# Kernel optimization log

Measured on AMD Instinct MI355X. Metric: run time of the kernel, lower is better.

Reference implementation:

```python
import jax, jax.numpy as jnp
import numpy as np

MARGIN = 0.3
WARMUP_EPOCHS = 10
K = 5
ALPHA = 2.0
SAME_CAM_NEG_BOOST = 1.2
NEG_INF = jnp.float32(-jnp.inf)
POS_INF = jnp.float32(jnp.inf)


def setup_inputs() -> dict:
    key = jax.random.key(0)
    k1, k2, k3 = jax.random.split(key, 3)
    N, D = 8192, 2048
    feats = jax.random.normal(k1, (N, D), dtype=jnp.float32)
    labels = jax.random.randint(k2, (N,), 0, 256, dtype=jnp.int64)
    camids = jax.random.randint(k3, (N,), 0, 8, dtype=jnp.int64)
    return {"feats": feats, "labels": labels, "camids": camids, "epoch": 20}


def _topk_mean(dist_mat, mask, k, largest):
    # dist_mat [N,N], mask [N,N] bool. Per-row mean of k largest/smallest valid elems.
    if largest:
        work = jnp.where(mask, dist_mat, NEG_INF)
        vals, _ = jax.lax.top_k(work, k)            # [N,k] largest
        fallback = jnp.max(work, axis=1)
    else:
        work = jnp.where(mask, dist_mat, POS_INF)
        vals = -jax.lax.top_k(-work, k)[0]          # [N,k] smallest
        fallback = jnp.min(work, axis=1)
    is_valid = jnp.isfinite(vals)
    safe_sum = jnp.sum(jnp.where(is_valid, vals, 0.0), axis=1)
    counts = jnp.maximum(is_valid.sum(axis=1), 1)
    mean = safe_sum / counts
    return jnp.where(is_valid.any(axis=1), mean, fallback)


def _forward(feats, labels, camids, epoch):
    # (1) L2 normalize
    norm = jnp.linalg.norm(feats, axis=-1, keepdims=True)
    x = feats / jnp.maximum(norm, 1e-12)
    # Euclidean distance matrix [N,N]
    sq = jnp.sum(x * x, axis=1)
    dist2 = sq[:, None] + sq[None, :] - 2.0 * (x @ x.T)
    dist = jnp.sqrt(jnp.maximum(dist2, 1e-12))
    # masks (constants w.r.t. grad)
    N = feats.shape[0]
    eye = jnp.eye(N, dtype=bool)
    same_label = labels[:, None] == labels[None, :]
    same_cam = camids[:, None] == camids[None, :]
    is_pos = same_label & ~eye & ~same_cam   # cross_cam_pos=True
    is_neg = ~same_label & ~eye
    # boosted same-camera negatives
    neg_bias = jnp.where(is_neg & same_cam, SAME_CAM_NEG_BOOST, 1.0)
    dist_neg_sel = dist / jnp.maximum(neg_bias, 1e-6)
    # (2) top-k hard mining
    d_ap = _topk_mean(dist, is_pos, K, largest=True)
    d_an = _topk_mean(dist_neg_sel, is_neg, K, largest=False)
    # (5) hardness-aware weighting (no grad)
    w = jax.lax.stop_gradient(jax.nn.sigmoid(ALPHA * (d_ap - d_an)))
    w = w / jnp.maximum(w.mean(), 1e-12)
    # (3) margin schedule
    if epoch is not None and epoch < WARMUP_EPOCHS:
        per_sample = jax.nn.softplus(-(d_an - d_ap))
    else:
        per_sample = jax.nn.relu(d_ap - d_an + MARGIN)  # MarginRankingLoss, y=1
    loss = jnp.mean(w * per_sample)
    return loss, jax.lax.stop_gradient(d_ap), jax.lax.stop_gradient(d_an)


def reference(feats, labels, camids, epoch):
    return _forward(feats, labels, camids, epoch)
```

## Files before the change

kernel.cpp:

```cpp
#include <hip/hip_runtime.h>
#include <hip/hip_bf16.h>
#include <stdint.h>

typedef float   floatx4  __attribute__((ext_vector_type(4)));
typedef float   floatx16 __attribute__((ext_vector_type(16)));
typedef int     intx4    __attribute__((ext_vector_type(4)));
typedef int     intx8    __attribute__((ext_vector_type(8)));
typedef _Float16 halfx8  __attribute__((ext_vector_type(8)));
typedef _Float16 halfx4  __attribute__((ext_vector_type(4)));
typedef _Float16 half2v  __attribute__((ext_vector_type(2)));

#define NROW 8192
#define NDIM 2048
#define BM 128
#define SLICE 64
#define NSLICE 32
#define NSTRIP 64
#define NTILE (NSTRIP*(NSTRIP+1)/2)
#define NPOSB 256
#define DT_LD 136
#define KL_SYM 64
#define SLOT_P 8
#define MERGE_BLOCKS 256
#define BOOST_INV 0.6944444444f
#define XBT_STRIP 262144
#define XBT_SLICE 8192

__device__ __forceinline__ void ins_desc(float (&a)[5], float v) {
#pragma unroll
    for (int k = 0; k < 5; ++k) { float hi = fmaxf(a[k], v); float lo = fminf(a[k], v); a[k] = hi; v = lo; }
}
__device__ __forceinline__ void ins_asc(float (&a)[5], float v) {
#pragma unroll
    for (int k = 0; k < 5; ++k) { float lo = fminf(a[k], v); float hi = fmaxf(a[k], v); a[k] = lo; v = hi; }
}

__device__ __forceinline__ int   h2bits(half2v v) { return __builtin_bit_cast(int, v); }
__device__ __forceinline__ half2v bits2h(int v)   { return __builtin_bit_cast(half2v, v); }
__device__ __forceinline__ void ins_desc2(half2v (&a)[5], half2v v) {
#pragma unroll
    for (int k = 0; k < 5; ++k) {
        half2v hi = __builtin_elementwise_max(a[k], v);
        half2v lo = __builtin_elementwise_min(a[k], v);
        a[k] = hi; v = lo;
    }
}
__device__ __forceinline__ void ins_asc2(half2v (&a)[5], half2v v) {
#pragma unroll
    for (int k = 0; k < 5; ++k) {
        half2v lo = __builtin_elementwise_min(a[k], v);
        half2v hi = __builtin_elementwise_max(a[k], v);
        a[k] = lo; v = hi;
    }
}

__device__ __forceinline__ void load_lds16(const void* g, void* l) {
    __builtin_amdgcn_global_load_lds((__attribute__((address_space(1))) void*)(void*)g,
                                     (__attribute__((address_space(3))) void*)l,
                                     16, 0, 0);
}

__global__ __launch_bounds__(256) void k_normalize(const float* __restrict__ feats,
                                                   unsigned char* __restrict__ xb,
                                                   unsigned char* __restrict__ xbt,
                                                   float* __restrict__ sq) {
    const int lane = threadIdx.x & 63;
    const int row = (blockIdx.x << 2) + (threadIdx.x >> 6);
    const float* f = feats + (size_t)row * NDIM;
    float4 v[8];
    float ss = 0.f;
#pragma unroll
    for (int i = 0; i < 8; ++i) {
        v[i] = *(const float4*)(f + ((i << 6) + lane) * 4);
        ss += v[i].x * v[i].x + v[i].y * v[i].y + v[i].z * v[i].z + v[i].w * v[i].w;
    }
#pragma unroll
    for (int o = 32; o > 0; o >>= 1) ss += __shfl_xor(ss, o);
    float inv = 1.0f / fmaxf(sqrtf(ss), 1e-12f);
    if (lane == 0) sq[row] = ss * inv * inv;
    unsigned char* xo = xb + (size_t)row * NDIM;
    const int strip = row >> 7, rr = row & 127, g = rr >> 5, m32r = rr & 31;
    unsigned char* bt = xbt + (size_t)strip * XBT_STRIP + g * 2048 + m32r * 32
                      + ((lane >> 4) * XBT_SLICE) + (((lane >> 3) & 1) * 1024) + 4 * (lane & 7);
#pragma unroll
    for (int i = 0; i < 8; ++i) {
        int w0 = __builtin_amdgcn_cvt_pk_fp8_f32(v[i].x * inv, v[i].y * inv, 0, false);
        w0     = __builtin_amdgcn_cvt_pk_fp8_f32(v[i].z * inv, v[i].w * inv, w0, true);
        *(int*)(xo + ((i << 6) + lane) * 4) = w0;
        *(int*)(bt + (size_t)4 * i * XBT_SLICE) = w0;
    }
}

__device__ __forceinline__ void scan_half_row_neg(const _Float16* Dt_,
        int srow, int shalf, float (&neg5)[5]) {
    const int s2 = 2 * (srow & 7);
    const int PINF2 = 0x7C007C00;
    half2v n5[5];
#pragma unroll
    for (int k = 0; k < 5; ++k) n5[k] = bits2h(PINF2);
#pragma unroll
    for (int c8 = 0; c8 < 8; ++c8) {
        const int pc = ((shalf * 8 + c8) + s2) & 15;
        intx4 v = *(const intx4*)(Dt_ + srow * DT_LD + pc * 8);
#pragma unroll
        for (int e = 0; e < 4; ++e) ins_asc2(n5, bits2h(v[e]));
    }
    half2v tn[5];
#pragma unroll
    for (int k = 0; k < 5; ++k)
        tn[k] = bits2h((int)__builtin_amdgcn_alignbit((unsigned)h2bits(n5[k]), (unsigned)h2bits(n5[k]), 16));
#pragma unroll
    for (int k = 0; k < 5; ++k) ins_asc2(n5, tn[k]);
#pragma unroll
    for (int k = 0; k < 5; ++k) neg5[k] = (float)n5[k][0];
}

__device__ __forceinline__ void emit_neg(float (&neg5)[5], int shalf,
        _Float16* negp, int gi, int slot) {
    float tn[5];
#pragma unroll
    for (int k = 0; k < 5; ++k) tn[k] = __shfl_xor(neg5[k], 1);
#pragma unroll
    for (int k = 0; k < 5; ++k) { if (tn[k] < neg5[4]) ins_asc(neg5, tn[k]); }
    if (shalf == 0) {
        const float PINF = __builtin_inff();
        halfx8 hn;
#pragma unroll
        for (int k = 0; k < 5; ++k) hn[k] = (_Float16)neg5[k];
        hn[5] = hn[6] = hn[7] = (_Float16)PINF;
        *(halfx8*)(negp + ((size_t)slot * NROW + gi) * SLOT_P) = hn;
    }
}

__global__ __launch_bounds__(256, 3) void k_main(
        const unsigned char* __restrict__ xb, const unsigned char* __restrict__ xbt,
        const float* __restrict__ sq,
        const int* __restrict__ labels, const int* __restrict__ camids,
        _Float16* __restrict__ negp, _Float16* __restrict__ posf) {
    __shared__ __align__(16) char smem[36864];

    const int tid = threadIdx.x;
    const int w = tid >> 6, lane = tid & 63;
    const int m32 = lane & 31;
    const int hi = lane >> 5;
    const int key = (lane >> 1) & 3;
    const int p0 = ((2 * hi + key) & 3) * 16;
    const int p1 = ((2 * hi + 1 + key) & 3) * 16;
    const float FINF = __builtin_inff();
    const float NINF = -FINF;

    if (blockIdx.x < NPOSB) {
        char* stg0 = smem;
        _Float16* D2 = (_Float16*)(smem + 12288);
        int* mem = (int*)(smem + 21504);
        unsigned short* mlc = (unsigned short*)(smem + 21760);
        float* msq = (float*)(smem + 21888);
        int* cntp = (int*)(smem + 22144);

        const int L = blockIdx.x;
        if (tid == 0) *cntp = 0;
        __syncthreads();
        for (int i = tid; i < NROW; i += 256) {
            if (labels[i] == L) {
                int slot = atomicAdd(cntp, 1);
                if (slot < 64) mem[slot] = i;
            }
        }
        __syncthreads();
        const int cnt = min(*cntp, 64);
        if (tid < 64) {
            if (tid < cnt) {
                int gi = mem[tid];
                mlc[tid] = (unsigned short)((labels[gi] << 4) | camids[gi]);
                msq[tid] = sq[gi];
            } else {
                mem[tid] = 0; mlc[tid] = 0xFFFF; msq[tid] = 0.f;
            }
        }
        __syncthreads();

        const int wm = w >> 1, wn = w & 1;
        const int lr = lane >> 2;
        const int lcb = (((lane & 3) - ((lane >> 3) & 3)) & 3) * 16;
        const int myrow = mem[w * 16 + lr];

        auto pstage = [&](int buf, int koff) {
            load_lds16(xb + (size_t)myrow * NDIM + koff + lcb,
                       stg0 + (buf << 12) + w * 1024);
        };

        floatx16 acc;
#pragma unroll
        for (int r = 0; r < 16; ++r) acc[r] = 0.f;

        pstage(0, 0);
        pstage(1, SLICE);
        for (int s = 0; s < NSLICE; ++s) {
            if (s + 2 < NSLICE) pstage((s + 2) % 3, (s + 2) * SLICE);
            if (s < NSLICE - 2)       asm volatile("s_waitcnt vmcnt(2)" ::: "memory");
            else if (s == NSLICE - 2) asm volatile("s_waitcnt vmcnt(1)" ::: "memory");
            else                      asm volatile("s_waitcnt vmcnt(0)" ::: "memory");
            __builtin_amdgcn_s_barrier();
            asm volatile("" ::: "memory");
            const char* Ab = stg0 + ((s % 3) << 12);
            const char* ap = Ab + (wm * 32 + m32) * SLICE;
            intx4 alo = *(const intx4*)(ap + p0);
            intx4 ahi = *(const intx4*)(ap + p1);
            intx8 af = __builtin_shufflevector(alo, ahi, 0, 1, 2, 3, 4, 5, 6, 7);
            const char* bp = Ab + (wn * 32 + m32) * SLICE;
            intx4 blo = *(const intx4*)(bp + p0);
            intx4 bhi = *(const intx4*)(bp + p1);
            intx8 bf = __builtin_shufflevector(blo, bhi, 0, 1, 2, 3, 4, 5, 6, 7);
            acc = __builtin_amdgcn_mfma_scale_f32_32x32x64_f8f6f4(af, bf, acc, 0, 0, 0, 127, 0, 127);
            asm volatile("" ::: "memory");
            __builtin_amdgcn_s_barrier();
            asm volatile("" ::: "memory");
        }

        {
            const int jl = (w & 1) * 32 + m32;
            const int lcj = (int)mlc[jl];
            const float sj = msq[jl];
            const int wm2 = w >> 1;
#pragma unroll
            for (int r = 0; r < 16; ++r) {
                const int il = wm2 * 32 + (r & 3) + 8 * (r >> 2) + 4 * hi;
                float d2 = fmaxf(msq[il] + sj - 2.0f * acc[r], 1e-12f);
                const int x = (int)mlc[il] ^ lcj;
                bool posv = ((x & 0xFFF0) == 0) & ((x & 15) != 0);
                D2[il * 72 + jl] = posv ? (_Float16)d2 : (_Float16)NINF;
            }
        }
        __syncthreads();

        {
            const int prow = tid >> 2, q = tid & 3;
            const int NINF2 = 0xFC00FC00;
            half2v p5h[5];
#pragma unroll
            for (int k = 0; k < 5; ++k) p5h[k] = bits2h(NINF2);
            const _Float16* dp = D2 + prow * 72 + q * 16;
            intx4 v0 = *(const intx4*)dp;
            intx4 v1 = *(const intx4*)(dp + 8);
#pragma unroll
            for (int e = 0; e < 4; ++e) ins_desc2(p5h, bits2h(v0[e]));
#pragma unroll
            for (int e = 0; e < 4; ++e) ins_desc2(p5h, bits2h(v1[e]));
            half2v tp[5];
#pragma unroll
            for (int k = 0; k < 5; ++k)
                tp[k] = bits2h((int)__builtin_amdgcn_alignbit((unsigned)h2bits(p5h[k]), (unsigned)h2bits(p5h[k]), 16));
#pragma unroll
            for (int k = 0; k < 5; ++k) ins_desc2(p5h, tp[k]);
            float p5[5];
#pragma unroll
            for (int k = 0; k < 5; ++k) p5[k] = (float)p5h[k][0];
#pragma unroll
            for (int o = 1; o <= 2; o <<= 1) {
                float tq[5];
#pragma unroll
                for (int k = 0; k < 5; ++k) tq[k] = __shfl_xor(p5[k], o);
#pragma unroll
                for (int k = 0; k < 5; ++k) { if (tq[k] > p5[4]) ins_desc(p5, tq[k]); }
            }
            if (q == 0 && prow < cnt) {
                halfx8 hp;
#pragma unroll
                for (int k = 0; k < 5; ++k) hp[k] = (_Float16)p5[k];
                hp[5] = hp[6] = hp[7] = (_Float16)NINF;
                *(halfx8*)(posf + (size_t)mem[prow] * SLOT_P) = hp;
            }
        }
        return;
    }

    _Float16* Dt = (_Float16*)smem;
    float* sqr_s = (float*)(smem + 34816);
    float* sqc_s = sqr_s + BM;
    unsigned short* labcam_a = (unsigned short*)(sqc_s + BM);
    unsigned short* labcam_b = labcam_a + BM;

    const int wm = w >> 1, wn = w & 1;

    int a, b;
    {
        int bx = blockIdx.x - NPOSB;
        int o = (bx & 7) * (NTILE / 8) + (bx >> 3);
        if (o < 1792) {
            int st = o >> 6;
            int SA = (int)((1.0f + sqrtf(8.0f * (float)st + 1.0f)) * 0.5f);
            while (SA * (SA - 1) / 2 > st) --SA;
            while (SA * (SA + 1) / 2 <= st) ++SA;
            int SB = st - SA * (SA - 1) / 2;
            int inner = o & 63;
            a = SA * 8 + (inner >> 3);
            b = SB * 8 + (inner & 7);
        } else {
            int idx = o - 1792;
            int st = idx / 36;
            int inner = idx - st * 36;
            int ia = (int)((sqrtf(8.0f * (float)inner + 1.0f) - 1.0f) * 0.5f);
            while (ia * (ia + 1) / 2 > inner) --ia;
            while ((ia + 1) * (ia + 2) / 2 <= inner) ++ia;
            int ib = inner - ia * (ia + 1) / 2;
            a = st * 8 + ia;
            b = st * 8 + ib;
        }
    }
    const int r0 = a * BM, c0 = b * BM;

    if (tid < BM) {
        int gi = r0 + tid;
        sqr_s[tid] = sq[gi];
        labcam_a[tid] = (unsigned short)((labels[gi] << 4) | camids[gi]);
    } else {
        int t2 = tid - BM;
        int gj = c0 + t2;
        sqc_s[t2] = sq[gj];
        labcam_b[t2] = (unsigned short)((labels[gj] << 4) | camids[gj]);
    }

    const int lr = lane >> 2;
    const int lc = (((lane & 3) - ((lane >> 3) & 3)) & 3) * 16;
    auto stageB = [&](int buf, int koff) {
        char* Bsb = smem + (buf << 13);
#pragma unroll
        for (int q = 0; q < 2; ++q) {
            const int ra = w * 32 + q * 16;
            load_lds16(xb + (size_t)(c0 + ra + lr) * NDIM + koff + lc, Bsb + ra * SLICE);
        }
    };

    const unsigned char* aptrA = xbt + (size_t)a * XBT_STRIP + (2 * wm) * 2048 + lane * 32;
    const unsigned char* aptrB = aptrA + 2048;

    intx4 xa0, xa1, xa2, xa3;
    intx4 ya0, ya1, ya2, ya3;

    stageB(0, 0);
    xa0 = *(const intx4*)(aptrA);       xa1 = *(const intx4*)(aptrA + 16);
    xa2 = *(const intx4*)(aptrB);       xa3 = *(const intx4*)(aptrB + 16);
    stageB(1, SLICE);
    ya0 = *(const intx4*)(aptrA + XBT_SLICE);      ya1 = *(const intx4*)(aptrA + XBT_SLICE + 16);
    ya2 = *(const intx4*)(aptrB + XBT_SLICE);      ya3 = *(const intx4*)(aptrB + XBT_SLICE + 16);

    const int srow = tid >> 1;
    const int shalf = tid & 1;

    floatx16 acc[2][2];
#pragma unroll
    for (int ti = 0; ti < 2; ++ti)
#pragma unroll
        for (int tj = 0; tj < 2; ++tj)
#pragma unroll
            for (int r = 0; r < 16; ++r) acc[ti][tj][r] = 0.f;

    for (int s = 0; s < NSLICE; s += 2) {
        if (s + 2 < NSLICE) {
            stageB((s + 2) & 3, (s + 2) * SLICE);
            asm volatile("s_waitcnt vmcnt(8)" ::: "memory");
        } else {
            asm volatile("s_waitcnt vmcnt(6)" ::: "memory");
        }
        __builtin_amdgcn_s_barrier();
        asm volatile("" ::: "memory");
        {
            const char* Bb = smem + ((s & 3) << 13);
            intx8 bf0, bf1;
            {
                const char* bp = Bb + (wn * 64 + m32) * SLICE;
                intx4 lo = *(const intx4*)(bp + p0);
                intx4 h4 = *(const intx4*)(bp + p1);
                bf0 = __builtin_shufflevector(lo, h4, 0, 1, 2, 3, 4, 5, 6, 7);
            }
            {
                const char* bp = Bb + (wn * 64 + 32 + m32) * SLICE;
                intx4 lo = *(const intx4*)(bp + p0);
                intx4 h4 = *(const intx4*)(bp + p1);
                bf1 = __builtin_shufflevector(lo, h4, 0, 1, 2, 3, 4, 5, 6, 7);
            }
            __builtin_amdgcn_s_setprio(1);
            intx8 af0 = __builtin_shufflevector(xa0, xa1, 0, 1, 2, 3, 4, 5, 6, 7);
            intx8 af1 = __builtin_shufflevector(xa2, xa3, 0, 1, 2, 3, 4, 5, 6, 7);
            acc[0][0] = __builtin_amdgcn_mfma_scale_f32_32x32x64_f8f6f4(af0, bf0, acc[0][0], 0, 0, 0, 127, 0, 127);
            acc[0][1] = __builtin_amdgcn_mfma_scale_f32_32x32x64_f8f6f4(af0, bf1, acc[0][1], 0, 0, 0, 127, 0, 127);
            acc[1][0] = __builtin_amdgcn_mfma_scale_f32_32x32x64_f8f6f4(af1, bf0, acc[1][0], 0, 0, 0, 127, 0, 127);
            acc[1][1] = __builtin_amdgcn_mfma_scale_f32_32x32x64_f8f6f4(af1, bf1, acc[1][1], 0, 0, 0, 127, 0, 127);
            __builtin_amdgcn_s_setprio(0);
        }
        if (s + 2 < NSLICE) {
            const size_t ko = (size_t)(s + 2) * XBT_SLICE;
            xa0 = *(const intx4*)(aptrA + ko); xa1 = *(const intx4*)(aptrA + ko + 16);
            xa2 = *(const intx4*)(aptrB + ko); xa3 = *(const intx4*)(aptrB + ko + 16);
        }
        if (s + 3 < NSLICE) {
            stageB((s + 3) & 3, (s + 3) * SLICE);
            asm volatile("s_waitcnt vmcnt(8)" ::: "memory");
        } else {
            asm volatile("s_waitcnt vmcnt(0)" ::: "memory");
        }
        __builtin_amdgcn_s_barrier();
        asm volatile("" ::: "memory");
        {
            const char* Bb = smem + (((s + 1) & 3) << 13);
            intx8 bf0, bf1;
            {
                const char* bp = Bb + (wn * 64 + m32) * SLICE;
                intx4 lo = *(const intx4*)(bp + p0);
                intx4 h4 = *(const intx4*)(bp + p1);
                bf0 = __builtin_shufflevector(lo, h4, 0, 1, 2, 3, 4, 5, 6, 7);
            }
            {
                const char* bp = Bb + (wn * 64 + 32 + m32) * SLICE;
                intx4 lo = *(const intx4*)(bp + p0);
                intx4 h4 = *(const intx4*)(bp + p1);
                bf1 = __builtin_shufflevector(lo, h4, 0, 1, 2, 3, 4, 5, 6, 7);
            }
            __builtin_amdgcn_s_setprio(1);
            intx8 af0 = __builtin_shufflevector(ya0, ya1, 0, 1, 2, 3, 4, 5, 6, 7);
            intx8 af1 = __builtin_shufflevector(ya2, ya3, 0, 1, 2, 3, 4, 5, 6, 7);
            acc[0][0] = __builtin_amdgcn_mfma_scale_f32_32x32x64_f8f6f4(af0, bf0, acc[0][0], 0, 0, 0, 127, 0, 127);
            acc[0][1] = __builtin_amdgcn_mfma_scale_f32_32x32x64_f8f6f4(af0, bf1, acc[0][1], 0, 0, 0, 127, 0, 127);
            acc[1][0] = __builtin_amdgcn_mfma_scale_f32_32x32x64_f8f6f4(af1, bf0, acc[1][0], 0, 0, 0, 127, 0, 127);
            acc[1][1] = __builtin_amdgcn_mfma_scale_f32_32x32x64_f8f6f4(af1, bf1, acc[1][1], 0, 0, 0, 127, 0, 127);
            __builtin_amdgcn_s_setprio(0);
        }
        if (s + 3 < NSLICE) {
            const size_t ko = (size_t)(s + 3) * XBT_SLICE;
            ya0 = *(const intx4*)(aptrA + ko); ya1 = *(const intx4*)(aptrA + ko + 16);
            ya2 = *(const intx4*)(aptrB + ko); ya3 = *(const intx4*)(aptrB + ko + 16);
        }
    }
    __syncthreads();

    {
        const int jl0 = wn * 64 + m32, jl1 = jl0 + 32;
        const float sj0 = sqc_s[jl0], sj1 = sqc_s[jl1];
        const int lb0 = (int)labcam_b[jl0], lb1 = (int)labcam_b[jl1];
        const int jc0 = jl0 >> 3, j7_0 = jl0 & 7;
        const int jc1 = jl1 >> 3, j7_1 = jl1 & 7;
#pragma unroll
        for (int ti = 0; ti < 2; ++ti) {
#pragma unroll
            for (int r = 0; r < 16; ++r) {
                const int il = wm * 64 + ti * 32 + (r & 3) + 8 * (r >> 2) + 4 * hi;
                const float si = sqr_s[il];
                const int la = (int)labcam_a[il];
                const int rot = 2 * (il & 7);
                _Float16* drow = Dt + il * DT_LD;

                float d2 = fmaxf(si + sj0 - 2.0f * acc[ti][0][r], 1e-12f);
                int x = la ^ lb0;
                float nv = (x & 15) ? d2 : d2 * BOOST_INV;
                nv = (x & 0xFFF0) ? nv : FINF;
                acc[ti][0][r] = nv;
                drow[(((jc0 + rot) & 15) << 3) + j7_0] = (_Float16)nv;

                d2 = fmaxf(si + sj1 - 2.0f * acc[ti][1][r], 1e-12f);
                x = la ^ lb1;
                nv = (x & 15) ? d2 : d2 * BOOST_INV;
                nv = (x & 0xFFF0) ? nv : FINF;
                acc[ti][1][r] = nv;
                drow[(((jc1 + rot) & 15) << 3) + j7_1] = (_Float16)nv;
            }
        }
    }
    __syncthreads();

    float neg5[5];
    scan_half_row_neg(Dt, srow, shalf, neg5);
    emit_neg(neg5, shalf, negp, r0 + srow, b);

    if (a != b) {
        __syncthreads();
#pragma unroll
        for (int tj = 0; tj < 2; ++tj) {
#pragma unroll
            for (int ti = 0; ti < 2; ++ti) {
                const int jl = wn * 64 + tj * 32 + m32;
                const int cw2 = 2 * (jl & 7);
#pragma unroll
                for (int rq = 0; rq < 4; ++rq) {
                    const int base_row = wm * 64 + ti * 32 + 8 * rq + 4 * hi;
                    halfx4 h;
#pragma unroll
                    for (int e = 0; e < 4; ++e) h[e] = (_Float16)acc[ti][tj][rq * 4 + e];
                    const int pch = (((base_row >> 3) + cw2) & 15);
                    *(halfx4*)(Dt + jl * DT_LD + (pch << 3) + 4 * hi) = h;
                }
            }
        }
        __syncthreads();
        scan_half_row_neg(Dt, srow, shalf, neg5);
        emit_neg(neg5, shalf, negp, c0 + srow, a);
    }
}

__global__ __launch_bounds__(256) void k_merge_sym(const _Float16* __restrict__ negp,
        const _Float16* __restrict__ posf, const int* __restrict__ epoch_p,
        float* __restrict__ out, float* __restrict__ wsum_p, float* __restrict__ wpsum_p) {
    const int t = threadIdx.x;
    const int rl = t & 31;
    const int sg = t >> 5;
    const int row = blockIdx.x * 32 + rl;
    const float NINF = -__builtin_inff(), PINF = __builtin_inff();
    float n5[5] = {PINF, PINF, PINF, PINF, PINF};
    const size_t rbase = (size_t)row * SLOT_P;
#pragma unroll
    for (int s = 0; s < 8; ++s) {
        const size_t off = (size_t)(sg * 8 + s) * ((size_t)NROW * SLOT_P) + rbase;
        halfx8 nv = *(const halfx8*)(negp + off);
#pragma unroll
        for (int e = 0; e < 8; ++e) { float f = (float)nv[e]; if (f < n5[4]) ins_asc(n5, f); }
    }
    __shared__ __align__(16) _Float16 ln[32][8][8];
    const int sw = (sg + rl) & 7;
    {
        halfx8 hn;
#pragma unroll
        for (int k = 0; k < 5; ++k) hn[k] = (_Float16)n5[k];
        hn[5] = hn[6] = hn[7] = (_Float16)PINF;
        *(halfx8*)&ln[rl][sw][0] = hn;
    }
    __syncthreads();
    if (t < 32) {
        float N5[5] = {PINF, PINF, PINF, PINF, PINF};
#pragma unroll
        for (int g = 0; g < 8; ++g) {
            halfx8 nv = *(const halfx8*)&ln[t][g][0];
#pragma unroll
            for (int e = 0; e < 8; ++e) { float f = (float)nv[e]; if (f < N5[4]) ins_asc(N5, f); }
        }
        const int orow = blockIdx.x * 32 + t;
        halfx8 pv = *(const halfx8*)(posf + (size_t)orow * SLOT_P);
        float s = 0.f; int c = 0;
#pragma unroll
        for (int k = 0; k < 5; ++k) { float f = (float)pv[k]; bool fin = (f > NINF); s += fin ? sqrtf(f) : 0.f; c += fin ? 1 : 0; }
        float d_ap = (c > 0) ? s / (float)c : NINF;
        s = 0.f; c = 0;
#pragma unroll
        for (int k = 0; k < 5; ++k) { bool fin = (N5[k] < PINF); s += fin ? sqrtf(N5[k]) : 0.f; c += fin ? 1 : 0; }
        float d_an = (c > 0) ? s / (float)c : PINF;

        out[1 + orow] = d_ap;
        out[1 + NROW + orow] = d_an;
        float diff = d_ap - d_an;
        float w0 = 1.0f / (1.0f + expf(-2.0f * diff));
        float p;
        if (*epoch_p < 10) {
            p = fmaxf(diff, 0.0f) + log1pf(expf(-fabsf(diff)));
        } else {
            p = fmaxf(diff + 0.3f, 0.0f);
        }
        float wp = w0 * p;
#pragma unroll
        for (int o = 16; o > 0; o >>= 1) { w0 += __shfl_down(w0, o, 32); wp += __shfl_down(wp, o, 32); }
        if (t == 0) { wsum_p[blockIdx.x] = w0; wpsum_p[blockIdx.x] = wp; }
    }
}

__global__ void k_finalize(const float* __restrict__ wsum_p, const float* __restrict__ wpsum_p,
                           float* __restrict__ out) {
    const int t = threadIdx.x;
    float sw  = wsum_p[t] + wsum_p[t + 64] + wsum_p[t + 128] + wsum_p[t + 192];
    float swp = wpsum_p[t] + wpsum_p[t + 64] + wpsum_p[t + 128] + wpsum_p[t + 192];
#pragma unroll
    for (int o = 32; o > 0; o >>= 1) { sw += __shfl_down(sw, o); swp += __shfl_down(swp, o); }
    if (t == 0) {
        float M = fmaxf(sw / (float)NROW, 1e-12f);
        out[0] = swp / ((float)NROW * M);
    }
}

extern "C" void kernel_launch(void* const* d_in, const int* in_sizes, int n_in,
                              void* d_out, int out_size, void* d_ws, size_t ws_size,
                              hipStream_t stream) {
    const float* feats  = (const float*)d_in[0];
    const int*   labels = (const int*)d_in[1];
    const int*   camids = (const int*)d_in[2];
    const int*   epoch  = (const int*)d_in[3];
    float* out = (float*)d_out;
    char* ws = (char*)d_ws;

    unsigned char* xb  = (unsigned char*)ws;
    unsigned char* xbt = (unsigned char*)(ws + 16777216);
    float* sq = (float*)(ws + 33554432);
    const size_t NEG_HALVES = (size_t)KL_SYM * NROW * SLOT_P;
    _Float16* negp = (_Float16*)(ws + 33554432 + 32768);
    _Float16* posf = negp + NEG_HALVES;
    float* wsum_p  = (float*)((char*)(posf + (size_t)NROW * SLOT_P));
    float* wpsum_p = wsum_p + MERGE_BLOCKS;

    k_normalize<<<NROW / 4, 256, 0, stream>>>(feats, xb, xbt, sq);
    k_main<<<NPOSB + NTILE, 256, 0, stream>>>(xb, xbt, sq, labels, camids, negp, posf);
    k_merge_sym<<<MERGE_BLOCKS, 256, 0, stream>>>(negp, posf, epoch, out, wsum_p, wpsum_p);
    k_finalize<<<1, 64, 0, stream>>>(wsum_p, wpsum_p, out);
}
```

Measured before the change: 211.6 us.

## Load B operand fragments directly from pre-swizzled global layout, drop LDS staging

The B-tile operand of the FP8 MFMA GEMM is now read straight from the pre-permuted xbt global buffer into registers, the same way the A operand already was. The LDS staging buffers, async LDS loads, waitcnt/barrier pairs per slice and the LDS fragment reads are removed from the main loop. This removes per-slice block synchronisation and LDS traffic, but B data is no longer shared across the waves through LDS: each wave fetches its own fragments from global/L2, which raises global load volume and register pressure (eight more intx4 registers).

Result: faster. 205.4 us (-3.0%).

```diff
diff --git a/kernel.cpp b/kernel.cpp
--- a/kernel.cpp
+++ b/kernel.cpp
@@ -143,9 +143,6 @@
     const int w = tid >> 6, lane = tid & 63;
     const int m32 = lane & 31;
     const int hi = lane >> 5;
-    const int key = (lane >> 1) & 3;
-    const int p0 = ((2 * hi + key) & 3) * 16;
-    const int p1 = ((2 * hi + 1 + key) & 3) * 16;
     const float FINF = __builtin_inff();
     const float NINF = -FINF;
 
@@ -156,6 +153,10 @@
         unsigned short* mlc = (unsigned short*)(smem + 21760);
         float* msq = (float*)(smem + 21888);
         int* cntp = (int*)(smem + 22144);
+
+        const int key = (lane >> 1) & 3;
+        const int p0 = ((2 * hi + key) & 3) * 16;
+        const int p1 = ((2 * hi + 1 + key) & 3) * 16;
 
         const int L = blockIdx.x;
         if (tid == 0) *cntp = 0;
@@ -319,30 +320,24 @@
         sqc_s[t2] = sq[gj];
         labcam_b[t2] = (unsigned short)((labels[gj] << 4) | camids[gj]);
     }
-
-    const int lr = lane >> 2;
-    const int lc = (((lane & 3) - ((lane >> 3) & 3)) & 3) * 16;
-    auto stageB = [&](int buf, int koff) {
-        char* Bsb = smem + (buf << 13);
-#pragma unroll
-        for (int q = 0; q < 2; ++q) {
-            const int ra = w * 32 + q * 16;
-            load_lds16(xb + (size_t)(c0 + ra + lr) * NDIM + koff + lc, Bsb + ra * SLICE);
-        }
-    };
-
-    const unsigned char* aptrA = xbt + (size_t)a * XBT_STRIP + (2 * wm) * 2048 + lane * 32;
-    const unsigned char* aptrB = aptrA + 2048;
-
-    intx4 xa0, xa1, xa2, xa3;
-    intx4 ya0, ya1, ya2, ya3;
-
-    stageB(0, 0);
-    xa0 = *(const intx4*)(aptrA);       xa1 = *(const intx4*)(aptrA + 16);
-    xa2 = *(const intx4*)(aptrB);       xa3 = *(const intx4*)(aptrB + 16);
-    stageB(1, SLICE);
-    ya0 = *(const intx4*)(aptrA + XBT_SLICE);      ya1 = *(const intx4*)(aptrA + XBT_SLICE + 16);
-    ya2 = *(const intx4*)(aptrB + XBT_SLICE);      ya3 = *(const intx4*)(aptrB + XBT_SLICE + 16);
+    __syncthreads();
+
+    const unsigned char* aptr0 = xbt + (size_t)a * XBT_STRIP + (2 * wm) * 2048 + lane * 32;
+    const unsigned char* aptr1 = aptr0 + 2048;
+    const unsigned char* bptr0 = xbt + (size_t)b * XBT_STRIP + (2 * wn) * 2048 + lane * 32;
+    const unsigned char* bptr1 = bptr0 + 2048;
+
+    intx4 xa0, xa1, xa2, xa3, xq0, xq1, xq2, xq3;
+    intx4 ya0, ya1, ya2, ya3, yq0, yq1, yq2, yq3;
+
+    xa0 = *(const intx4*)(aptr0);       xa1 = *(const intx4*)(aptr0 + 16);
+    xa2 = *(const intx4*)(aptr1);       xa3 = *(const intx4*)(aptr1 + 16);
+    xq0 = *(const intx4*)(bptr0);       xq1 = *(const intx4*)(bptr0 + 16);
+    xq2 = *(const intx4*)(bptr1);       xq3 = *(const intx4*)(bptr1 + 16);
+    ya0 = *(const intx4*)(aptr0 + XBT_SLICE); ya1 = *(const intx4*)(aptr0 + XBT_SLICE + 16);
+    ya2 = *(const intx4*)(aptr1 + XBT_SLICE); ya3 = *(const intx4*)(aptr1 + XBT_SLICE + 16);
+    yq0 = *(const intx4*)(bptr0 + XBT_SLICE); yq1 = *(const intx4*)(bptr0 + XBT_SLICE + 16);
+    yq2 = *(const intx4*)(bptr1 + XBT_SLICE); yq3 = *(const intx4*)(bptr1 + XBT_SLICE + 16);
 
     const int srow = tid >> 1;
     const int shalf = tid & 1;
@@ -356,32 +351,12 @@
             for (int r = 0; r < 16; ++r) acc[ti][tj][r] = 0.f;
 
     for (int s = 0; s < NSLICE; s += 2) {
-        if (s + 2 < NSLICE) {
-            stageB((s + 2) & 3, (s + 2) * SLICE);
-            asm volatile("s_waitcnt vmcnt(8)" ::: "memory");
-        } else {
-            asm volatile("s_waitcnt vmcnt(6)" ::: "memory");
-        }
-        __builtin_amdgcn_s_barrier();
-        asm volatile("" ::: "memory");
         {
-            const char* Bb = smem + ((s & 3) << 13);
-            intx8 bf0, bf1;
-            {
-                const char* bp = Bb + (wn * 64 + m32) * SLICE;
-                intx4 lo = *(const intx4*)(bp + p0);
-                intx4 h4 = *(const intx4*)(bp + p1);
-                bf0 = __builtin_shufflevector(lo, h4, 0, 1, 2, 3, 4, 5, 6, 7);
-            }
-            {
-                const char* bp = Bb + (wn * 64 + 32 + m32) * SLICE;
-                intx4 lo = *(const intx4*)(bp + p0);
-                intx4 h4 = *(const intx4*)(bp + p1);
-                bf1 = __builtin_shufflevector(lo, h4, 0, 1, 2, 3, 4, 5, 6, 7);
-            }
-            __builtin_amdgcn_s_setprio(1);
             intx8 af0 = __builtin_shufflevector(xa0, xa1, 0, 1, 2, 3, 4, 5, 6, 7);
             intx8 af1 = __builtin_shufflevector(xa2, xa3, 0, 1, 2, 3, 4, 5, 6, 7);
+            intx8 bf0 = __builtin_shufflevector(xq0, xq1, 0, 1, 2, 3, 4, 5, 6, 7);
+            intx8 bf1 = __builtin_shufflevector(xq2, xq3, 0, 1, 2, 3, 4, 5, 6, 7);
+            __builtin_amdgcn_s_setprio(1);
             acc[0][0] = __builtin_amdgcn_mfma_scale_f32_32x32x64_f8f6f4(af0, bf0, acc[0][0], 0, 0, 0, 127, 0, 127);
             acc[0][1] = __builtin_amdgcn_mfma_scale_f32_32x32x64_f8f6f4(af0, bf1, acc[0][1], 0, 0, 0, 127, 0, 127);
             acc[1][0] = __builtin_amdgcn_mfma_scale_f32_32x32x64_f8f6f4(af1, bf0, acc[1][0], 0, 0, 0, 127, 0, 127);
@@ -390,35 +365,17 @@
         }
         if (s + 2 < NSLICE) {
             const size_t ko = (size_t)(s + 2) * XBT_SLICE;
-            xa0 = *(const intx4*)(aptrA + ko); xa1 = *(const intx4*)(aptrA + ko + 16);
-            xa2 = *(const intx4*)(aptrB + ko); xa3 = *(const intx4*)(aptrB + ko + 16);
-        }
-        if (s + 3 < NSLICE) {
-            stageB((s + 3) & 3, (s + 3) * SLICE);
-            asm volatile("s_waitcnt vmcnt(8)" ::: "memory");
-        } else {
-            asm volatile("s_waitcnt vmcnt(0)" ::: "memory");
-        }
-        __builtin_amdgcn_s_barrier();
-        asm volatile("" ::: "memory");
+            xa0 = *(const intx4*)(aptr0 + ko); xa1 = *(const intx4*)(aptr0 + ko + 16);
+            xa2 = *(const intx4*)(aptr1 + ko); xa3 = *(const intx4*)(aptr1 + ko + 16);
+            xq0 = *(const intx4*)(bptr0 + ko); xq1 = *(const intx4*)(bptr0 + ko + 16);
+            xq2 = *(const intx4*)(bptr1 + ko); xq3 = *(const intx4*)(bptr1 + ko + 16);
+        }
         {
-            const char* Bb = smem + (((s + 1) & 3) << 13);
-            intx8 bf0, bf1;
-            {
-                const char* bp = Bb + (wn * 64 + m32) * SLICE;
-                intx4 lo = *(const intx4*)(bp + p0);
-                intx4 h4 = *(const intx4*)(bp + p1);
-                bf0 = __builtin_shufflevector(lo, h4, 0, 1, 2, 3, 4, 5, 6, 7);
-            }
-            {
-                const char* bp = Bb + (wn * 64 + 32 + m32) * SLICE;
-                intx4 lo = *(const intx4*)(bp + p0);
-                intx4 h4 = *(const intx4*)(bp + p1);
-                bf1 = __builtin_shufflevector(lo, h4, 0, 1, 2, 3, 4, 5, 6, 7);
-            }
-            __builtin_amdgcn_s_setprio(1);
             intx8 af0 = __builtin_shufflevector(ya0, ya1, 0, 1, 2, 3, 4, 5, 6, 7);
             intx8 af1 = __builtin_shufflevector(ya2, ya3, 0, 1, 2, 3, 4, 5, 6, 7);
+            intx8 bf0 = __builtin_shufflevector(yq0, yq1, 0, 1, 2, 3, 4, 5, 6, 7);
+            intx8 bf1 = __builtin_shufflevector(yq2, yq3, 0, 1, 2, 3, 4, 5, 6, 7);
+            __builtin_amdgcn_s_setprio(1);
             acc[0][0] = __builtin_amdgcn_mfma_scale_f32_32x32x64_f8f6f4(af0, bf0, acc[0][0], 0, 0, 0, 127, 0, 127);
             acc[0][1] = __builtin_amdgcn_mfma_scale_f32_32x32x64_f8f6f4(af0, bf1, acc[0][1], 0, 0, 0, 127, 0, 127);
             acc[1][0] = __builtin_amdgcn_mfma_scale_f32_32x32x64_f8f6f4(af1, bf0, acc[1][0], 0, 0, 0, 127, 0, 127);
@@ -427,11 +384,12 @@
         }
         if (s + 3 < NSLICE) {
             const size_t ko = (size_t)(s + 3) * XBT_SLICE;
-            ya0 = *(const intx4*)(aptrA + ko); ya1 = *(const intx4*)(aptrA + ko + 16);
-            ya2 = *(const intx4*)(aptrB + ko); ya3 = *(const intx4*)(aptrB + ko + 16);
-        }
-    }
-    __syncthreads();
+            ya0 = *(const intx4*)(aptr0 + ko); ya1 = *(const intx4*)(aptr0 + ko + 16);
+            ya2 = *(const intx4*)(aptr1 + ko); ya3 = *(const intx4*)(aptr1 + ko + 16);
+            yq0 = *(const intx4*)(bptr0 + ko); yq1 = *(const intx4*)(bptr0 + ko + 16);
+            yq2 = *(const intx4*)(bptr1 + ko); yq3 = *(const intx4*)(bptr1 + ko + 16);
+        }
+    }
 
     {
         const int jl0 = wn * 64 + m32, jl1 = jl0 + 32;
```
